# Performance work log

Measured on AMD Instinct MI355X. Metric: run time of the kernel, lower is better.

The kernel has to match this reference:

```python
import jax, jax.numpy as jnp
import numpy as np


def setup_inputs() -> dict:
    key = jax.random.key(0)
    ks = jax.random.split(key, 7)
    B, T, C, H = 4, 4096, 1024, 64
    x = jax.random.normal(ks[0], (B, T, C), dtype=jnp.float32)
    Wq = jax.random.normal(ks[1], (C, H), dtype=jnp.float32) * 0.02
    bq = jax.random.normal(ks[2], (H,), dtype=jnp.float32) * 0.02
    Wk = jax.random.normal(ks[3], (C, H), dtype=jnp.float32) * 0.02
    bk = jax.random.normal(ks[4], (H,), dtype=jnp.float32) * 0.02
    Wv = jax.random.normal(ks[5], (C, H), dtype=jnp.float32) * 0.02
    bv = jax.random.normal(ks[6], (H,), dtype=jnp.float32) * 0.02
    return {"x": x, "Wq": Wq, "bq": bq, "Wk": Wk, "bk": bk, "Wv": Wv, "bv": bv}


def reference(x, Wq, bq, Wk, bk, Wv, bv):
    B, T, C = x.shape
    q = x @ Wq + bq            # [B,T,H]
    k = x @ Wk + bk            # [B,T,H]
    v = x @ Wv + bv            # [B,T,H]
    # NOTE: original scales by C**-0.5 where C = n_embd (input dim), not head_size
    scale = jnp.asarray(C, x.dtype) ** -0.5
    wei = jnp.einsum('bth,bsh->bts', q, k) * scale   # [B,T,T]
    causal = jnp.tril(jnp.ones((T, T), dtype=bool))
    wei = jnp.where(causal, wei, -jnp.inf)
    wei = jax.nn.softmax(wei, axis=-1)
    out = jnp.einsum('bts,bsh->bth', wei, v)         # [B,T,H]
    return out
```

## Files before the change

kernel.cpp:

```cpp
#include <hip/hip_runtime.h>
#include <hip/hip_bf16.h>

#define T_DIM 4096
#define C_DIM 1024
#define H_DIM 64
#define B_DIM 4

typedef __attribute__((ext_vector_type(8))) short short8v;
typedef __attribute__((ext_vector_type(4))) float float4v;

__device__ __forceinline__ unsigned short f2bf(float f) {
    __hip_bfloat16 h = __float2bfloat16(f);
    return *reinterpret_cast<unsigned short*>(&h);
}

__device__ __forceinline__ int vperm(int t5) {
    return ((t5 & 12) << 1) | (t5 & 3) | ((t5 & 16) >> 2);
}

__device__ __forceinline__ int chunk_prefix(int t) {
    const int g = t >> 3;
    return t + 4 * g * (g - 1) + (t & 7) * g;
}

#define GLL16(gsrc, ldst)                                                         \
    __builtin_amdgcn_global_load_lds(                                             \
        (const __attribute__((address_space(1))) unsigned int*)(gsrc),            \
        (__attribute__((address_space(3))) unsigned int*)(ldst), 16, 0, 0)

__global__ __launch_bounds__(256) void wprep(
    const float* __restrict__ Wq, const float* __restrict__ Wk,
    const float* __restrict__ Wv, unsigned short* __restrict__ wt)
{
    __shared__ float tile[64][65];
    const int t  = threadIdx.x;
    const int m  = blockIdx.x >> 4;
    const int k0 = (blockIdx.x & 15) * 64;
    const float* __restrict__ W = (m == 0) ? Wq : (m == 1) ? Wk : Wv;

    const int kr = t >> 4, c4 = (t & 15) * 4;
#pragma unroll
    for (int j = 0; j < 4; ++j) {
        const int row = kr + j * 16;
        const float4 v = *(const float4*)(W + (size_t)(k0 + row) * 64 + c4);
        tile[row][c4 + 0] = v.x; tile[row][c4 + 1] = v.y;
        tile[row][c4 + 2] = v.z; tile[row][c4 + 3] = v.w;
    }
    __syncthreads();

    const int col = t >> 2, q = t & 3;
    short8v s0, s1;
#pragma unroll
    for (int j = 0; j < 8; ++j) s0[j] = (short)f2bf(tile[q * 16 + j][col]);
#pragma unroll
    for (int j = 0; j < 8; ++j) s1[j] = (short)f2bf(tile[q * 16 + 8 + j][col]);
    unsigned short* dst = wt + (size_t)(m * 64 + col) * 1024 + k0 + q * 16;
    *(short8v*)dst = s0;
    *(short8v*)(dst + 8) = s1;
}

__global__ __launch_bounds__(512, 2) void qkv_gemm(
    const float* __restrict__ x, const unsigned short* __restrict__ wt,
    const float* __restrict__ bq, const float* __restrict__ bk,
    const float* __restrict__ bv,
    unsigned short* __restrict__ qb, unsigned short* __restrict__ kmat,
    unsigned short* __restrict__ vP)
{
    __shared__ __align__(16) unsigned char lx[2][4096];
    __shared__ __align__(16) unsigned char lw[3][24576];

    const int t    = threadIdx.x;
    const int lane = t & 63;
    const int w    = t >> 6;
    const int l15  = lane & 15;
    const int g4   = lane >> 4;
    const int r0   = blockIdx.x * 32;

    const int rg  = w & 1;
    const int cgr = (w >> 1) & 1;
    const int kh  = w >> 2;

    const int srow  = t >> 4;
    const int sq    = t & 15;
    const int xbyte = srow * 128 + ((sq >> 1) ^ (srow & 7)) * 16 + (sq & 1) * 8;
    const float* __restrict__ xsrc = x + (size_t)(r0 + srow) * C_DIM + sq * 4;
    const int wgs = (t & 7) ^ ((t >> 3) & 7);
    const unsigned char* __restrict__ wB = (const unsigned char*)wt;

    float4v acc[6];
#pragma unroll
    for (int cg = 0; cg < 6; ++cg) acc[cg] = (float4v){0.f, 0.f, 0.f, 0.f};

#define WSTAGE(p, kb)                                                             \
    {                                                                             \
        _Pragma("unroll")                                                         \
        for (int i = 0; i < 3; ++i)                                               \
            GLL16(wB + (size_t)(i * 64 + (t >> 3)) * 2048 + (kb) * 128 + wgs * 16,\
                  &lw[p][(i * 512 + t) * 16]);                                    \
    }
#define XCVT_WRITE(p, v)                                                          \
    {                                                                             \
        __hip_bfloat162 c0_ = __float22bfloat162_rn(make_float2((v).x, (v).y));   \
        __hip_bfloat162 c1_ = __float22bfloat162_rn(make_float2((v).z, (v).w));   \
        unsigned int* d_ = (unsigned int*)&lx[p][xbyte];                          \
        d_[0] = *(unsigned int*)&c0_;                                             \
        d_[1] = *(unsigned int*)&c1_;                                             \
    }

    float4 xvA, xvB;

    {
        const float4 x0 = *(const float4*)xsrc;
        WSTAGE(0, 0);
        WSTAGE(1, 1);
        __builtin_amdgcn_sched_barrier(0);
        xvA = *(const float4*)(xsrc + 64);
        XCVT_WRITE(0, x0);
        asm volatile("s_waitcnt vmcnt(4) lgkmcnt(0)" ::: "memory");
        __builtin_amdgcn_s_barrier();
        __builtin_amdgcn_sched_barrier(0);
    }

    const int arow = rg * 16 + l15;
    const int axor = arow & 7;
    const int kg   = kh * 4 + g4;

#pragma unroll
    for (int kb = 0; kb < 14; ++kb) {
        const int p  = kb % 3;
        const int ps = (kb + 2) % 3;
        WSTAGE(ps, kb + 2);
        __builtin_amdgcn_sched_barrier(0);
        if ((kb & 1) == 0) xvB = *(const float4*)(xsrc + (kb + 2) * 64);
        else               xvA = *(const float4*)(xsrc + (kb + 2) * 64);

        const short8v af = *(const short8v*)&lx[kb & 1][arow * 128 + (kg ^ axor) * 16];
#pragma unroll
        for (int cg = 0; cg < 6; ++cg) {
            const int col = cgr * 96 + cg * 16 + l15;
            const short8v bf =
                *(const short8v*)&lw[p][col * 128 + ((kg ^ (col & 7))) * 16];
            acc[cg] = __builtin_amdgcn_mfma_f32_16x16x32_bf16(af, bf, acc[cg], 0, 0, 0);
        }

        if ((kb & 1) == 0) { XCVT_WRITE((kb + 1) & 1, xvA); }
        else               { XCVT_WRITE((kb + 1) & 1, xvB); }

        asm volatile("s_waitcnt vmcnt(4) lgkmcnt(0)" ::: "memory");
        __builtin_amdgcn_s_barrier();
        __builtin_amdgcn_sched_barrier(0);
    }
    {
        const short8v af = *(const short8v*)&lx[0][arow * 128 + (kg ^ axor) * 16];
#pragma unroll
        for (int cg = 0; cg < 6; ++cg) {
            const int col = cgr * 96 + cg * 16 + l15;
            const short8v bf =
                *(const short8v*)&lw[2][col * 128 + ((kg ^ (col & 7))) * 16];
            acc[cg] = __builtin_amdgcn_mfma_f32_16x16x32_bf16(af, bf, acc[cg], 0, 0, 0);
        }
        XCVT_WRITE(1, xvA);
        asm volatile("s_waitcnt vmcnt(0) lgkmcnt(0)" ::: "memory");
        __builtin_amdgcn_s_barrier();
        __builtin_amdgcn_sched_barrier(0);
    }
    {
        const short8v af = *(const short8v*)&lx[1][arow * 128 + (kg ^ axor) * 16];
#pragma unroll
        for (int cg = 0; cg < 6; ++cg) {
            const int col = cgr * 96 + cg * 16 + l15;
            const short8v bf =
                *(const short8v*)&lw[0][col * 128 + ((kg ^ (col & 7))) * 16];
            acc[cg] = __builtin_amdgcn_mfma_f32_16x16x32_bf16(af, bf, acc[cg], 0, 0, 0);
        }
    }
    __syncthreads();

    float* comm = (float*)lw;
    if (kh == 1) {
        const int base = ((w - 4) * 64 + lane) * 24;
#pragma unroll
        for (int cg = 0; cg < 6; ++cg)
#pragma unroll
            for (int e = 0; e < 4; ++e) comm[base + cg * 4 + e] = acc[cg][e];
    }
    __syncthreads();
    if (kh == 0) {
        const int base = (w * 64 + lane) * 24;
#pragma unroll
        for (int cg = 0; cg < 6; ++cg)
#pragma unroll
            for (int e = 0; e < 4; ++e) acc[cg][e] += comm[base + cg * 4 + e];

        const float qs = 0.03125f * 1.44269504088896f;
#pragma unroll
        for (int cg = 0; cg < 6; ++cg) {
            const int cabs = cgr * 96 + cg * 16 + l15;
            const int m    = cabs >> 6;
            const int h    = cabs & 63;
            const float bb = ((m == 0) ? bq : (m == 1) ? bk : bv)[h];
#pragma unroll
            for (int rr = 0; rr < 4; ++rr) {
                const int row = r0 + rg * 16 + 4 * g4 + rr;
                const float vv = acc[cg][rr] + bb;
                if (m == 0) {
                    qb[(size_t)row * 64 + h] = f2bf(vv * qs);
                } else if (m == 1) {
                    kmat[(size_t)row * 64 + h] = f2bf(vv);
                } else {
                    const int b_i = row >> 12;
                    const int tt  = row & 4095;
                    const int tp  = (tt & ~31) | vperm(tt & 31);
                    vP[((size_t)b_i * 64 + h) * T_DIM + tp] = f2bf(vv);
                }
            }
        }
    }
#undef WSTAGE
#undef XCVT_WRITE
}

__global__ __launch_bounds__(256, 4) void attn_part(
    const unsigned short* __restrict__ qb, const unsigned short* __restrict__ kmat,
    const unsigned short* __restrict__ vP, float* __restrict__ pO,
    float* __restrict__ pl)
{
    __shared__ __align__(16) unsigned char lk[3][4096];
    __shared__ __align__(16) unsigned char lv[3][4096];

    const int tid  = threadIdx.x;
    const int w    = tid >> 6;
    const int lane = tid & 63;
    const int l15  = lane & 15;
    const int g    = lane >> 4;

    const int b   = blockIdx.x & 3;
    const int idx = 287 - (blockIdx.x >> 2);
    int t = 0;
    for (int tt = 1; tt < 64; ++tt)
        if (chunk_prefix(tt) <= idx) t = tt;
    const int c    = idx - chunk_prefix(t);
    const int q0   = t * 64;
    const int kv_l = q0 + 64;
    const int d0   = c * 512;
    const int dend = (d0 + 512 < kv_l) ? (d0 + 512) : kv_l;
    const int ns   = (dend - d0) >> 5;
    const int slot = b * 288 + idx;

    const unsigned char* kB = (const unsigned char*)kmat + (size_t)b * T_DIM * 128;
    const unsigned char* vB = (const unsigned char*)vP + (size_t)b * 64 * T_DIM * 2;
    const int krow = tid >> 3, kdg = tid & 7;
    const int vh = tid >> 2, vdg = tid & 3;
    const unsigned char* ksrc = kB + krow * 128 + ((kdg ^ (krow & 7)) * 16);
    const unsigned char* vsrc = vB + (size_t)vh * 8192 + ((vdg ^ (vh & 3)) * 16);
    const int kdst = tid * 16;

#define STAGE(p, ss)                                                          \
    {                                                                         \
        const int off_ = d0 + (ss) * 32;                                      \
        GLL16(ksrc + (size_t)off_ * 128, &lk[p][kdst]);                       \
        GLL16(vsrc + (size_t)off_ * 2,   &lv[p][kdst]);                       \
    }

    const unsigned short* qrow = qb + ((size_t)b * T_DIM + q0 + 16 * w + l15) * 64;
    const short8v qf0 = *(const short8v*)(qrow + 8 * g);
    const short8v qf1 = *(const short8v*)(qrow + 32 + 8 * g);

    short8v kones;
#pragma unroll
    for (int j = 0; j < 8; ++j) kones[j] = (short)0x3F80;

    float4v acc[4];
    float4v accl = (float4v){0.f, 0.f, 0.f, 0.f};
#pragma unroll
    for (int f = 0; f < 4; ++f) acc[f] = (float4v){0.f, 0.f, 0.f, 0.f};

    const int qmax = q0 + 16 * w + 15;
    const int kxor = l15 & 7;
    const int vxor = l15 & 3;

    STAGE(0, 0);
    STAGE(1, (ns > 1) ? 1 : 0);
    asm volatile("s_waitcnt vmcnt(2)" ::: "memory");
    __builtin_amdgcn_s_barrier();

    int p = 0;
    for (int s = 0; s < ns; ++s) {
        const int ps = (p + 2 >= 3) ? (p - 1) : (p + 2);
        const int sn = (s + 2 < ns) ? (s + 2) : (ns - 1);
        STAGE(ps, sn);

        const int kv0 = d0 + s * 32;
        if (kv0 <= qmax) {
            const short8v ka0 = *(const short8v*)&lk[p][(l15 * 8 + (g ^ kxor)) * 16];
            const short8v ka1 = *(const short8v*)&lk[p][(l15 * 8 + ((4 + g) ^ kxor)) * 16];
            const short8v ka2 = *(const short8v*)&lk[p][((16 + l15) * 8 + (g ^ kxor)) * 16];
            const short8v ka3 = *(const short8v*)&lk[p][((16 + l15) * 8 + ((4 + g) ^ kxor)) * 16];
            short8v vb[4];
#pragma unroll
            for (int f = 0; f < 4; ++f)
                vb[f] = *(const short8v*)&lv[p][((f * 16 + l15) * 4 + (g ^ vxor)) * 16];

            const float4v z = (float4v){0.f, 0.f, 0.f, 0.f};
            float4v slo = __builtin_amdgcn_mfma_f32_16x16x32_bf16(ka0, qf0, z, 0, 0, 0);
            slo = __builtin_amdgcn_mfma_f32_16x16x32_bf16(ka1, qf1, slo, 0, 0, 0);
            float4v shi = __builtin_amdgcn_mfma_f32_16x16x32_bf16(ka2, qf0, z, 0, 0, 0);
            shi = __builtin_amdgcn_mfma_f32_16x16x32_bf16(ka3, qf1, shi, 0, 0, 0);

            float pl_[4], ph_[4];
            if (kv0 + 31 <= q0 + 16 * w) {
#pragma unroll
                for (int r = 0; r < 4; ++r) {
                    pl_[r] = exp2f(slo[r]);
                    ph_[r] = exp2f(shi[r]);
                }
            } else {
                const int qabs = q0 + 16 * w + l15;
#pragma unroll
                for (int r = 0; r < 4; ++r) {
                    const int kvlo = kv0 + 4 * g + r;
                    pl_[r] = (kvlo <= qabs) ? exp2f(slo[r]) : 0.f;
                    ph_[r] = (kvlo + 16 <= qabs) ? exp2f(shi[r]) : 0.f;
                }
            }
            short8v pa;
            {
                unsigned int* pu = (unsigned int*)&pa;
                __hip_bfloat162 c0 = __float22bfloat162_rn(make_float2(pl_[0], pl_[1]));
                __hip_bfloat162 c1 = __float22bfloat162_rn(make_float2(pl_[2], pl_[3]));
                __hip_bfloat162 c2 = __float22bfloat162_rn(make_float2(ph_[0], ph_[1]));
                __hip_bfloat162 c3 = __float22bfloat162_rn(make_float2(ph_[2], ph_[3]));
                pu[0] = *(unsigned int*)&c0;
                pu[1] = *(unsigned int*)&c1;
                pu[2] = *(unsigned int*)&c2;
                pu[3] = *(unsigned int*)&c3;
            }
#pragma unroll
            for (int f = 0; f < 4; ++f)
                acc[f] = __builtin_amdgcn_mfma_f32_16x16x32_bf16(pa, vb[f], acc[f], 0, 0, 0);
            accl = __builtin_amdgcn_mfma_f32_16x16x32_bf16(pa, kones, accl, 0, 0, 0);
        }

        asm volatile("s_waitcnt vmcnt(2) lgkmcnt(0)" ::: "memory");
        __builtin_amdgcn_s_barrier();
        p = (p + 1 >= 3) ? 0 : (p + 1);
    }

    float* po = pO + (size_t)slot * 4096 + (size_t)(16 * w) * 64;
#pragma unroll
    for (int f = 0; f < 4; ++f)
#pragma unroll
        for (int r = 0; r < 4; ++r)
            po[(4 * g + r) * 64 + f * 16 + l15] = acc[f][r];
    if (l15 == 0) {
#pragma unroll
        for (int r = 0; r < 4; ++r)
            pl[(size_t)slot * 64 + 16 * w + 4 * g + r] = accl[r];
    }
#undef STAGE
}

__global__ __launch_bounds__(256) void attn_comb(
    const float* __restrict__ pO, const float* __restrict__ pl,
    float* __restrict__ out)
{
    const int tid  = blockIdx.x * 256 + threadIdx.x;
    const int row  = tid >> 4;
    const int h4   = (tid & 15) * 4;
    const int b    = row >> 12;
    const int brow = row & 4095;
    const int t    = brow >> 6;
    const int rr   = brow & 63;
    const int nc   = 1 + (t >> 3);
    const int base = b * 288 + chunk_prefix(t);

    const float* src  = pO + (size_t)base * 4096 + rr * 64 + h4;
    const float* lsrc = pl + (size_t)base * 64 + rr;
    float4 o = make_float4(0.f, 0.f, 0.f, 0.f);
    float l = 0.f;
    for (int c = 0; c < nc; ++c) {
        const float4 s = *(const float4*)(src + (size_t)c * 4096);
        o.x += s.x; o.y += s.y; o.z += s.z; o.w += s.w;
        l += lsrc[(size_t)c * 64];
    }
    const float inv = 1.f / l;
    o.x *= inv; o.y *= inv; o.z *= inv; o.w *= inv;
    *(float4*)(out + (size_t)row * 64 + h4) = o;
}

extern "C" void kernel_launch(void* const* d_in, const int* in_sizes, int n_in,
                              void* d_out, int out_size, void* d_ws, size_t ws_size,
                              hipStream_t stream) {
    const float* x  = (const float*)d_in[0];
    const float* Wq = (const float*)d_in[1];
    const float* bq = (const float*)d_in[2];
    const float* Wk = (const float*)d_in[3];
    const float* bk = (const float*)d_in[4];
    const float* Wv = (const float*)d_in[5];
    const float* bv = (const float*)d_in[6];
    float* out = (float*)d_out;

    char* ws = (char*)d_ws;
    unsigned short* qb   = (unsigned short*)(ws);
    unsigned short* kmat = (unsigned short*)(ws + (2u << 20));
    unsigned short* vP   = (unsigned short*)(ws + (4u << 20));
    unsigned short* wt   = (unsigned short*)(ws + (6u << 20));
    float*          pO   = (float*)(ws + (8u << 20));
    float*          pl   = (float*)(ws + (8u << 20) + 18874368u);

    wprep<<<48, 256, 0, stream>>>(Wq, Wk, Wv, wt);
    qkv_gemm<<<512, 512, 0, stream>>>(x, wt, bq, bk, bv, qb, kmat, vP);
    attn_part<<<1152, 256, 0, stream>>>(qb, kmat, vP, pO, pl);
    attn_comb<<<1024, 256, 0, stream>>>(pO, pl, out);
}
```

Baseline: 56.83 us.

## Load QKV GEMM operands directly from global memory with 4-way K split

Drops the LDS-staged, triple-buffered pipeline in the QKV projection GEMM. Each wave now reads x rows and bf16 weights straight from global memory into MFMA fragments, with the K dimension split four ways across waves and reduced through shared memory. Each wave covers two row groups so one weight fragment feeds two MFMAs, and launch bounds are raised to allow more resident blocks. This trades the explicit async prefetch and LDS reuse for more occupancy and less barrier synchronisation, at the risk of uncoalesced and repeated global reads of x and the weights.

```diff
diff --git a/kernel.cpp b/kernel.cpp
--- a/kernel.cpp
+++ b/kernel.cpp
@@ -12,6 +12,20 @@
 __device__ __forceinline__ unsigned short f2bf(float f) {
     __hip_bfloat16 h = __float2bfloat16(f);
     return *reinterpret_cast<unsigned short*>(&h);
+}
+
+__device__ __forceinline__ short8v pack8(float4 a, float4 b) {
+    short8v r;
+    unsigned int* u = (unsigned int*)&r;
+    __hip_bfloat162 c0 = __float22bfloat162_rn(make_float2(a.x, a.y));
+    __hip_bfloat162 c1 = __float22bfloat162_rn(make_float2(a.z, a.w));
+    __hip_bfloat162 c2 = __float22bfloat162_rn(make_float2(b.x, b.y));
+    __hip_bfloat162 c3 = __float22bfloat162_rn(make_float2(b.z, b.w));
+    u[0] = *(unsigned int*)&c0;
+    u[1] = *(unsigned int*)&c1;
+    u[2] = *(unsigned int*)&c2;
+    u[3] = *(unsigned int*)&c3;
+    return r;
 }
 
 __device__ __forceinline__ int vperm(int t5) {
@@ -59,15 +73,14 @@
     *(short8v*)(dst + 8) = s1;
 }
 
-__global__ __launch_bounds__(512, 2) void qkv_gemm(
+__global__ __launch_bounds__(512, 4) void qkv_gemm(
     const float* __restrict__ x, const unsigned short* __restrict__ wt,
     const float* __restrict__ bq, const float* __restrict__ bk,
     const float* __restrict__ bv,
     unsigned short* __restrict__ qb, unsigned short* __restrict__ kmat,
     unsigned short* __restrict__ vP)
 {
-    __shared__ __align__(16) unsigned char lx[2][4096];
-    __shared__ __align__(16) unsigned char lw[3][24576];
+    __shared__ float comm[6][64][48];
 
     const int t    = threadIdx.x;
     const int lane = t & 63;
@@ -76,148 +89,89 @@
     const int g4   = lane >> 4;
     const int r0   = blockIdx.x * 32;
 
-    const int rg  = w & 1;
-    const int cgr = (w >> 1) & 1;
-    const int kh  = w >> 2;
-
-    const int srow  = t >> 4;
-    const int sq    = t & 15;
-    const int xbyte = srow * 128 + ((sq >> 1) ^ (srow & 7)) * 16 + (sq & 1) * 8;
-    const float* __restrict__ xsrc = x + (size_t)(r0 + srow) * C_DIM + sq * 4;
-    const int wgs = (t & 7) ^ ((t >> 3) & 7);
-    const unsigned char* __restrict__ wB = (const unsigned char*)wt;
-
-    float4v acc[6];
-#pragma unroll
-    for (int cg = 0; cg < 6; ++cg) acc[cg] = (float4v){0.f, 0.f, 0.f, 0.f};
-
-#define WSTAGE(p, kb)                                                             \
-    {                                                                             \
-        _Pragma("unroll")                                                         \
-        for (int i = 0; i < 3; ++i)                                               \
-            GLL16(wB + (size_t)(i * 64 + (t >> 3)) * 2048 + (kb) * 128 + wgs * 16,\
-                  &lw[p][(i * 512 + t) * 16]);                                    \
-    }
-#define XCVT_WRITE(p, v)                                                          \
-    {                                                                             \
-        __hip_bfloat162 c0_ = __float22bfloat162_rn(make_float2((v).x, (v).y));   \
-        __hip_bfloat162 c1_ = __float22bfloat162_rn(make_float2((v).z, (v).w));   \
-        unsigned int* d_ = (unsigned int*)&lx[p][xbyte];                          \
-        d_[0] = *(unsigned int*)&c0_;                                             \
-        d_[1] = *(unsigned int*)&c1_;                                             \
-    }
-
-    float4 xvA, xvB;
-
-    {
-        const float4 x0 = *(const float4*)xsrc;
-        WSTAGE(0, 0);
-        WSTAGE(1, 1);
-        __builtin_amdgcn_sched_barrier(0);
-        xvA = *(const float4*)(xsrc + 64);
-        XCVT_WRITE(0, x0);
-        asm volatile("s_waitcnt vmcnt(4) lgkmcnt(0)" ::: "memory");
-        __builtin_amdgcn_s_barrier();
-        __builtin_amdgcn_sched_barrier(0);
-    }
-
-    const int arow = rg * 16 + l15;
-    const int axor = arow & 7;
-    const int kg   = kh * 4 + g4;
-
-#pragma unroll
-    for (int kb = 0; kb < 14; ++kb) {
-        const int p  = kb % 3;
-        const int ps = (kb + 2) % 3;
-        WSTAGE(ps, kb + 2);
-        __builtin_amdgcn_sched_barrier(0);
-        if ((kb & 1) == 0) xvB = *(const float4*)(xsrc + (kb + 2) * 64);
-        else               xvA = *(const float4*)(xsrc + (kb + 2) * 64);
-
-        const short8v af = *(const short8v*)&lx[kb & 1][arow * 128 + (kg ^ axor) * 16];
+    const int cgr = w & 1;
+    const int kq  = w >> 1;
+
+    const float* __restrict__ xr0 =
+        x + (size_t)(r0 + l15) * C_DIM + kq * 256 + 8 * g4;
+    const float* __restrict__ xr1 = xr0 + 16 * C_DIM;
+    const unsigned short* __restrict__ wb =
+        wt + kq * 256 + 8 * g4;
+
+    float4v acc[2][6];
+#pragma unroll
+    for (int rgi = 0; rgi < 2; ++rgi)
+#pragma unroll
+        for (int cg = 0; cg < 6; ++cg) acc[rgi][cg] = (float4v){0.f, 0.f, 0.f, 0.f};
+
+#pragma unroll
+    for (int kb = 0; kb < 8; ++kb) {
+        const float4 a00 = *(const float4*)(xr0 + kb * 32);
+        const float4 a01 = *(const float4*)(xr0 + kb * 32 + 4);
+        const float4 a10 = *(const float4*)(xr1 + kb * 32);
+        const float4 a11 = *(const float4*)(xr1 + kb * 32 + 4);
+        const short8v af0 = pack8(a00, a01);
+        const short8v af1 = pack8(a10, a11);
 #pragma unroll
         for (int cg = 0; cg < 6; ++cg) {
-            const int col = cgr * 96 + cg * 16 + l15;
-            const short8v bf =
-                *(const short8v*)&lw[p][col * 128 + ((kg ^ (col & 7))) * 16];
-            acc[cg] = __builtin_amdgcn_mfma_f32_16x16x32_bf16(af, bf, acc[cg], 0, 0, 0);
+            const short8v bf = *(const short8v*)(
+                wb + (size_t)(cgr * 96 + cg * 16 + l15) * 1024 + kb * 32);
+            acc[0][cg] = __builtin_amdgcn_mfma_f32_16x16x32_bf16(af0, bf, acc[0][cg], 0, 0, 0);
+            acc[1][cg] = __builtin_amdgcn_mfma_f32_16x16x32_bf16(af1, bf, acc[1][cg], 0, 0, 0);
         }
-
-        if ((kb & 1) == 0) { XCVT_WRITE((kb + 1) & 1, xvA); }
-        else               { XCVT_WRITE((kb + 1) & 1, xvB); }
-
-        asm volatile("s_waitcnt vmcnt(4) lgkmcnt(0)" ::: "memory");
-        __builtin_amdgcn_s_barrier();
-        __builtin_amdgcn_sched_barrier(0);
-    }
-    {
-        const short8v af = *(const short8v*)&lx[0][arow * 128 + (kg ^ axor) * 16];
-#pragma unroll
-        for (int cg = 0; cg < 6; ++cg) {
-            const int col = cgr * 96 + cg * 16 + l15;
-            const short8v bf =
-                *(const short8v*)&lw[2][col * 128 + ((kg ^ (col & 7))) * 16];
-            acc[cg] = __builtin_amdgcn_mfma_f32_16x16x32_bf16(af, bf, acc[cg], 0, 0, 0);
+    }
+
+    if (kq > 0) {
+        float* c = &comm[w - 2][lane][0];
+#pragma unroll
+        for (int rgi = 0; rgi < 2; ++rgi)
+#pragma unroll
+            for (int cg = 0; cg < 6; ++cg)
+#pragma unroll
+                for (int e = 0; e < 4; ++e)
+                    c[(rgi * 6 + cg) * 4 + e] = acc[rgi][cg][e];
+    }
+    __syncthreads();
+    if (kq == 0) {
+#pragma unroll
+        for (int j = 0; j < 3; ++j) {
+            const float* c = &comm[j * 2 + cgr][lane][0];
+#pragma unroll
+            for (int rgi = 0; rgi < 2; ++rgi)
+#pragma unroll
+                for (int cg = 0; cg < 6; ++cg)
+#pragma unroll
+                    for (int e = 0; e < 4; ++e)
+                        acc[rgi][cg][e] += c[(rgi * 6 + cg) * 4 + e];
         }
-        XCVT_WRITE(1, xvA);
-        asm volatile("s_waitcnt vmcnt(0) lgkmcnt(0)" ::: "memory");
-        __builtin_amdgcn_s_barrier();
-        __builtin_amdgcn_sched_barrier(0);
-    }
-    {
-        const short8v af = *(const short8v*)&lx[1][arow * 128 + (kg ^ axor) * 16];
-#pragma unroll
-        for (int cg = 0; cg < 6; ++cg) {
-            const int col = cgr * 96 + cg * 16 + l15;
-            const short8v bf =
-                *(const short8v*)&lw[0][col * 128 + ((kg ^ (col & 7))) * 16];
-            acc[cg] = __builtin_amdgcn_mfma_f32_16x16x32_bf16(af, bf, acc[cg], 0, 0, 0);
-        }
-    }
-    __syncthreads();
-
-    float* comm = (float*)lw;
-    if (kh == 1) {
-        const int base = ((w - 4) * 64 + lane) * 24;
-#pragma unroll
-        for (int cg = 0; cg < 6; ++cg)
-#pragma unroll
-            for (int e = 0; e < 4; ++e) comm[base + cg * 4 + e] = acc[cg][e];
-    }
-    __syncthreads();
-    if (kh == 0) {
-        const int base = (w * 64 + lane) * 24;
-#pragma unroll
-        for (int cg = 0; cg < 6; ++cg)
-#pragma unroll
-            for (int e = 0; e < 4; ++e) acc[cg][e] += comm[base + cg * 4 + e];
 
         const float qs = 0.03125f * 1.44269504088896f;
 #pragma unroll
-        for (int cg = 0; cg < 6; ++cg) {
-            const int cabs = cgr * 96 + cg * 16 + l15;
-            const int m    = cabs >> 6;
-            const int h    = cabs & 63;
-            const float bb = ((m == 0) ? bq : (m == 1) ? bk : bv)[h];
-#pragma unroll
-            for (int rr = 0; rr < 4; ++rr) {
-                const int row = r0 + rg * 16 + 4 * g4 + rr;
-                const float vv = acc[cg][rr] + bb;
-                if (m == 0) {
-                    qb[(size_t)row * 64 + h] = f2bf(vv * qs);
-                } else if (m == 1) {
-                    kmat[(size_t)row * 64 + h] = f2bf(vv);
-                } else {
-                    const int b_i = row >> 12;
-                    const int tt  = row & 4095;
-                    const int tp  = (tt & ~31) | vperm(tt & 31);
-                    vP[((size_t)b_i * 64 + h) * T_DIM + tp] = f2bf(vv);
+        for (int rgi = 0; rgi < 2; ++rgi) {
+#pragma unroll
+            for (int cg = 0; cg < 6; ++cg) {
+                const int cabs = cgr * 96 + cg * 16 + l15;
+                const int m    = cabs >> 6;
+                const int h    = cabs & 63;
+                const float bb = ((m == 0) ? bq : (m == 1) ? bk : bv)[h];
+#pragma unroll
+                for (int rr = 0; rr < 4; ++rr) {
+                    const int row = r0 + rgi * 16 + 4 * g4 + rr;
+                    const float vv = acc[rgi][cg][rr] + bb;
+                    if (m == 0) {
+                        qb[(size_t)row * 64 + h] = f2bf(vv * qs);
+                    } else if (m == 1) {
+                        kmat[(size_t)row * 64 + h] = f2bf(vv);
+                    } else {
+                        const int b_i = row >> 12;
+                        const int tt  = row & 4095;
+                        const int tp  = (tt & ~31) | vperm(tt & 31);
+                        vP[((size_t)b_i * 64 + h) * T_DIM + tp] = f2bf(vv);
+                    }
                 }
             }
         }
     }
-#undef WSTAGE
-#undef XCVT_WRITE
 }
 
 __global__ __launch_bounds__(256, 4) void attn_part(
```

After: 91.66 us. 1.61x slower.
